# Kernel optimization log

Hardware: AMD Instinct MI355X
Metric: run time of the kernel (lower is better)

## Reference

```python
import jax, jax.numpy as jnp
import numpy as np

N_NODES, N_EDGES, N_GRAPHS = 20000, 640000, 256
D_IN, H1, H2, H3, L, H4, ED = 7, 128, 128, 64, 16, 64, 1


def _gat_conv(x, src, dst, edge_attr, W, att_s, att_d, We, att_e, b):
    """PyG GATConv (heads=1, concat=True, edge_dim=ED, add_self_loops=True,
    fill_value='mean' for self-loop edge attrs, negative_slope=0.2)."""
    n = x.shape[0]
    h = x @ W                                  # [N, F]
    a_s = h @ att_s                            # [N]
    a_d = h @ att_d                            # [N]
    # append self loops; self-loop edge attr = mean of edge attrs
    loop = jnp.arange(n)
    src_f = jnp.concatenate([src, loop])
    dst_f = jnp.concatenate([dst, loop])
    ea_mean = edge_attr.mean(axis=0, keepdims=True)
    ea = jnp.concatenate([edge_attr, jnp.broadcast_to(ea_mean, (n, edge_attr.shape[1]))], axis=0)
    a_e = (ea @ We) @ att_e                    # [E+N]
    logits = jax.nn.leaky_relu(a_s[src_f] + a_d[dst_f] + a_e, 0.2)
    # neighborhood softmax over incoming edges of each dst node
    m = jax.ops.segment_max(logits, dst_f, num_segments=n)
    ex = jnp.exp(logits - m[dst_f])
    denom = jax.ops.segment_sum(ex, dst_f, num_segments=n)
    alpha = ex / denom[dst_f]                  # [E+N]
    out = jax.ops.segment_sum(alpha[:, None] * h[src_f], dst_f, num_segments=n)
    return out + b


def _branch(x, edge_index, edge_col, params):
    src, dst = edge_index[0], edge_index[1]
    for p in params:  # fixed 3 layers
        x = jax.nn.elu(_gat_conv(x, src, dst, edge_col, *p))
        # dropout p=0.2 is identity in eval mode
    return x


def _mean_pool(x, batch, num_graphs):
    s = jax.ops.segment_sum(x, batch, num_segments=num_graphs)
    cnt = jax.ops.segment_sum(jnp.ones((x.shape[0],), x.dtype), batch, num_segments=num_graphs)
    return s / jnp.maximum(cnt, 1.0)[:, None]


def setup_inputs() -> dict:
    key = jax.random.key(0)
    ks = jax.random.split(key, 40)
    inp = {
        "x1": jax.random.normal(ks[0], (N_NODES, D_IN), jnp.float32),
        "x2": jax.random.normal(ks[1], (N_NODES, D_IN), jnp.float32),
        "edge_index1": jax.random.randint(ks[2], (2, N_EDGES), 0, N_NODES),
        "edge_index2": jax.random.randint(ks[3], (2, N_EDGES), 0, N_NODES),
        "batch1": jnp.sort(jax.random.randint(ks[4], (N_NODES,), 0, N_GRAPHS)),
        "batch2": jnp.sort(jax.random.randint(ks[5], (N_NODES,), 0, N_GRAPHS)),
        "x_norm2_1": jax.random.normal(ks[6], (N_GRAPHS, L), jnp.float32),
        "x_norm2_2": jax.random.normal(ks[7], (N_GRAPHS, L), jnp.float32),
        "edge_col1": jax.random.normal(ks[8], (N_EDGES, ED), jnp.float32),
        "edge_col2": jax.random.normal(ks[9], (N_EDGES, ED), jnp.float32),
    }
    dims = [(D_IN, H1), (H1, H2), (H2, H3)]
    k = 10
    for i, (fi, fo) in enumerate(dims, start=1):
        sc = 1.0 / np.sqrt(fi)
        inp[f"W{i}"] = jax.random.normal(ks[k], (fi, fo), jnp.float32) * sc; k += 1
        inp[f"as{i}"] = jax.random.normal(ks[k], (fo,), jnp.float32) * 0.1; k += 1
        inp[f"ad{i}"] = jax.random.normal(ks[k], (fo,), jnp.float32) * 0.1; k += 1
        inp[f"We{i}"] = jax.random.normal(ks[k], (ED, fo), jnp.float32); k += 1
        inp[f"ae{i}"] = jax.random.normal(ks[k], (fo,), jnp.float32) * 0.1; k += 1
        inp[f"b{i}"] = jnp.zeros((fo,), jnp.float32); k += 1
    inp["linW"] = jax.random.normal(ks[k], (H3 + L, H4), jnp.float32) * (1.0 / np.sqrt(H3 + L)); k += 1
    inp["linb"] = jnp.zeros((H4,), jnp.float32)
    return inp


def reference(x1, x2, edge_index1, edge_index2, batch1, batch2, x_norm2_1, x_norm2_2,
              edge_col1, edge_col2,
              W1, as1, ad1, We1, ae1, b1,
              W2, as2, ad2, We2, ae2, b2,
              W3, as3, ad3, We3, ae3, b3,
              linW, linb):
    params = [(W1, as1, ad1, We1, ae1, b1),
              (W2, as2, ad2, We2, ae2, b2),
              (W3, as3, ad3, We3, ae3, b3)]
    h1 = _branch(x1, edge_index1, edge_col1, params)
    h2 = _branch(x2, edge_index2, edge_col2, params)
    g1 = _mean_pool(h1, batch1, N_GRAPHS)
    g2 = _mean_pool(h2, batch2, N_GRAPHS)
    o1 = jnp.concatenate([g1, x_norm2_1], axis=1) @ linW + linb
    o2 = jnp.concatenate([g2, x_norm2_2], axis=1) @ linW + linb
    return (o1, o2)
```

## Files before the change

### kernel.cpp

```cpp
#include <hip/hip_runtime.h>
#include <hip/hip_bf16.h>
#include <hip/hip_fp16.h>

#define N_NODES 20000
#define N_EDGES 640000
#define N_GRAPHS 256
#define NBUCK 313
#define NBP 320
#define NA 160
#define NC 160
#define EPC 4000
#define DCAP 2560
#define CURP 16

typedef short bf16v __attribute__((ext_vector_type(8)));
typedef float f32x4 __attribute__((ext_vector_type(4)));
typedef float f32x2 __attribute__((ext_vector_type(2)));

__device__ __forceinline__ float leaky02(float x){ return x > 0.f ? x : 0.2f*x; }
__device__ __forceinline__ float eluf(float x){ return x > 0.f ? x : (__expf(x) - 1.f); }
__device__ __forceinline__ unsigned short f2bf(float x){
  __hip_bfloat16 t = __float2bfloat16(x);
  return *reinterpret_cast<unsigned short*>(&t);
}
__device__ __forceinline__ float bflo(unsigned int u){ return __uint_as_float(u << 16); }
__device__ __forceinline__ float bfhi(unsigned int u){ return __uint_as_float(u & 0xffff0000u); }
__device__ __forceinline__ void pkfma(f32x2& acc, f32x2 a, f32x2 b){
  asm volatile("v_pk_fma_f32 %0, %1, %2, %0" : "+v"(acc) : "v"(a), "v"(b));
}

__global__ __launch_bounds__(256) void binA_kernel(
    const int* __restrict__ ei0, const int* __restrict__ ei1,
    const float* __restrict__ ec0, const float* __restrict__ ec1,
    int* __restrict__ gcount, float* __restrict__ part)
{
  int b = blockIdx.y;
  const int* dstp = (b ? ei1 : ei0) + N_EDGES;
  const float* ec = b ? ec1 : ec0;
  __shared__ int hist[NBUCK];
  int tid = threadIdx.x;
  for (int j = tid; j < NBUCK; j += 256) hist[j] = 0;
  __syncthreads();
  float v = 0.f;
  for (int i = blockIdx.x*256 + tid; i < N_EDGES; i += NA*256){
    atomicAdd(&hist[dstp[i] >> 6], 1);
    v += ec[i];
  }
  __syncthreads();
  for (int j = tid; j < NBUCK; j += 256)
    if (hist[j]) atomicAdd(&gcount[b*NBP + j], hist[j]);
  for (int o = 32; o; o >>= 1) v += __shfl_down(v, o);
  __shared__ float wr[4];
  int lane = tid & 63, wv = tid >> 6;
  if (lane == 0) wr[wv] = v;
  __syncthreads();
  if (tid == 0) part[b*NA + blockIdx.x] = wr[0]+wr[1]+wr[2]+wr[3];
}

__global__ __launch_bounds__(512) void binB_kernel(
    const int* __restrict__ gcount, const float* __restrict__ part,
    const int* __restrict__ bat0, const int* __restrict__ bat1,
    const float* __restrict__ We1, const float* __restrict__ ae1,
    const float* __restrict__ We2, const float* __restrict__ ae2,
    const float* __restrict__ We3, const float* __restrict__ ae3,
    int* __restrict__ bcur, int* __restrict__ cbase,
    int* __restrict__ gb, float* __restrict__ scal, int* __restrict__ rowp)
{
  int b = blockIdx.x;
  int tid = threadIdx.x;
  if (b == 0){
    int wv = tid >> 6, lane = tid & 63;
    if (wv < 3){
      const float* We = wv==0 ? We1 : (wv==1 ? We2 : We3);
      const float* ae = wv==0 ? ae1 : (wv==1 ? ae2 : ae3);
      int F = (wv==2) ? 64 : 128;
      float s = 0.f;
      for (int i = lane; i < F; i += 64) s += We[i]*ae[i];
      for (int o = 32; o; o >>= 1) s += __shfl_down(s, o);
      if (lane == 0) scal[2+wv] = s;
    }
  }
  {
    float s = 0.f;
    for (int i = tid; i < NA; i += 512) s += part[b*NA + i];
    for (int o = 32; o; o >>= 1) s += __shfl_down(s, o);
    __shared__ float fr[8];
    if ((tid & 63) == 0) fr[tid >> 6] = s;
    __syncthreads();
    if (tid == 0){
      float t = 0.f;
      for (int i = 0; i < 8; ++i) t += fr[i];
      scal[b] = t;
    }
  }
  {
    const int* batch = b ? bat1 : bat0;
    int* gbb = gb + b*257;
    if (tid <= N_GRAPHS){
      int g = tid, lo = 0, hi = N_NODES;
      while (lo < hi){ int mid = (lo+hi) >> 1; if (batch[mid] < g) lo = mid+1; else hi = mid; }
      gbb[g] = lo;
    }
  }
  __shared__ int sc[512];
  int sz = (tid < NBUCK) ? gcount[b*NBP + tid] : 0;
  sc[tid] = sz;
  __syncthreads();
  for (int d = 1; d < 512; d <<= 1){
    int a2 = (tid >= d) ? sc[tid-d] : 0;
    __syncthreads();
    sc[tid] += a2;
    __syncthreads();
  }
  if (tid < NBUCK){
    int ecx = sc[tid] - sz;
    cbase[b*NBP + tid] = ecx;
    bcur[(b*NBUCK + tid)*CURP] = ecx;
  }
  if (tid == 0) rowp[b*(N_NODES+1) + N_NODES] = N_EDGES;
}

__global__ __launch_bounds__(256) void binC_kernel(
    const int* __restrict__ ei0, const int* __restrict__ ei1,
    const float* __restrict__ ec0, const float* __restrict__ ec1,
    int* __restrict__ bcur, uint2* __restrict__ stage)
{
  int b = blockIdx.y;
  const int* srcp = (b ? ei1 : ei0);
  const int* dstp = srcp + N_EDGES;
  const float* ec = b ? ec1 : ec0;
  int* bcurb = bcur + (size_t)b*NBUCK*CURP;
  uint2* stageb = stage + (size_t)b*N_EDGES;
  __shared__ uint2 recs[EPC];
  __shared__ int hist[NBUCK], rbase[NBUCK], rcur[NBUCK];
  int tid = threadIdx.x;
  for (int j = tid; j < NBUCK; j += 256){ hist[j] = 0; rcur[j] = 0; }
  __syncthreads();
  int e0 = blockIdx.x*EPC;
  for (int r = tid; r < EPC; r += 256){
    int i = e0 + r;
    int d = dstp[i];
    int bk = d >> 6;
    uint2 rec;
    rec.x = (unsigned)srcp[i] | ((unsigned)(d & 63) << 16);
    rec.y = ((unsigned)f2bf(ec[i]) << 16) | (unsigned)bk;
    recs[r] = rec;
    atomicAdd(&hist[bk], 1);
  }
  __syncthreads();
  for (int j = tid; j < NBUCK; j += 256){
    int h = hist[j];
    rbase[j] = h ? atomicAdd(&bcurb[j*CURP], h) : 0;
  }
  __syncthreads();
  for (int r = tid; r < EPC; r += 256){
    uint2 rc = recs[r];
    int bk = (int)(rc.y & 0xFFFFu);
    int p = rbase[bk] + atomicAdd(&rcur[bk], 1);
    stageb[p] = rc;
  }
}

__global__ __launch_bounds__(256) void binD_kernel(
    const uint2* __restrict__ stage, const int* __restrict__ gcount,
    const int* __restrict__ cbase,
    unsigned* __restrict__ final_, int* __restrict__ rowp)
{
  int b = blockIdx.y;
  int g = blockIdx.x;
  int tid = threadIdx.x;
  const uint2* stageb = stage + (size_t)b*N_EDGES;
  unsigned* finb = final_ + (size_t)b*N_EDGES;
  int* rowb = rowp + b*(N_NODES+1);
  int n = min(gcount[b*NBP + g], DCAP);
  int cb = cbase[b*NBP + g];
  __shared__ uint2 recs[DCAP];
  __shared__ int cnt64[64], cur64[64], off64[64];
  if (tid < 64) cnt64[tid] = 0;
  __syncthreads();
  for (int r = tid; r < n; r += 256){
    uint2 rc = stageb[cb + r];
    recs[r] = rc;
    atomicAdd(&cnt64[(rc.x >> 16) & 63], 1);
  }
  __syncthreads();
  if (tid == 0){
    int acc = 0;
    for (int dl = 0; dl < 64; ++dl){
      off64[dl] = acc; cur64[dl] = acc; acc += cnt64[dl];
    }
  }
  __syncthreads();
  int nd = min(64, N_NODES - g*64);
  if (tid < nd) rowb[g*64 + tid] = cb + off64[tid];
  for (int r = tid; r < n; r += 256){
    uint2 rc = recs[r];
    int dl = (rc.x >> 16) & 63;
    int p = atomicAdd(&cur64[dl], 1);
    finb[cb + p] = (rc.y & 0xFFFF0000u) | (rc.x & 0xFFFFu);
  }
}

template<int K, int F>
__global__ __launch_bounds__(256) void node_linear1_kernel(
    const float* __restrict__ x0, const float* __restrict__ x1,
    const float* __restrict__ W,
    const float* __restrict__ atts, const float* __restrict__ attd,
    unsigned short* __restrict__ hbAll, float* __restrict__ aSAll, float* __restrict__ aDAll)
{
  int b = blockIdx.y;
  const float* x = b ? x1 : x0;
  unsigned short* hb = hbAll + (size_t)b*N_NODES*128;
  float* a_s = aSAll + b*N_NODES;
  float* a_d = aDAll + b*N_NODES;
  constexpr int ROWS = 256 / F;
  __shared__ float Wl[K*F];
  __shared__ float xl[ROWS*K];
  __shared__ float swv[4], dwv[4];
  int tid = threadIdx.x;
  for (int i = tid; i < K*F; i += 256) Wl[i] = W[i];
  int f = tid % F;
  int lr = tid / F;
  float vs = atts[f], vd = attd[f];
  const int ntiles = (N_NODES + ROWS - 1)/ROWS;
  for (int t = blockIdx.x; t < ntiles; t += gridDim.x){
    int r0 = t*ROWS;
    __syncthreads();
    for (int i = tid; i < ROWS*K; i += 256){
      int r = i / K, k = i % K;
      int row = r0 + r;
      xl[i] = (row < N_NODES) ? x[row*K + k] : 0.f;
    }
    __syncthreads();
    float acc = 0.f;
    #pragma unroll
    for (int k = 0; k < K; ++k) acc += xl[lr*K + k] * Wl[k*F + f];
    int row = r0 + lr;
    if (row < N_NODES) hb[row*F + f] = f2bf(acc);
    float s = acc*vs, d = acc*vd;
    #pragma unroll
    for (int o = 32; o; o >>= 1){ s += __shfl_down(s, o); d += __shfl_down(d, o); }
    int wv = tid >> 6;
    if ((tid & 63) == 0){ swv[wv] = s; dwv[wv] = d; }
    __syncthreads();
    if (f == 0 && row < N_NODES){
      a_s[row] = swv[2*lr] + swv[2*lr+1];
      a_d[row] = dwv[2*lr] + dwv[2*lr+1];
    }
  }
}

template<int F>
__global__ __launch_bounds__(256) void gemm_mfma_kernel(
    const unsigned short* __restrict__ AAll, const float* __restrict__ W,
    const float* __restrict__ atts, const float* __restrict__ attd,
    unsigned short* __restrict__ hbAll, float* __restrict__ aSAll, float* __restrict__ aDAll)
{
  int b = blockIdx.y;
  const unsigned short* A = AAll + (size_t)b*N_NODES*128;
  unsigned short* hb = hbAll + (size_t)b*N_NODES*128;
  float* a_s = aSAll + b*N_NODES;
  float* a_d = aDAll + b*N_NODES;
  constexpr int NT = F/16;
  constexpr int KP = 136;
  __shared__ unsigned short Wb[F*KP];
  int tid = threadIdx.x;
  for (int idx = tid; idx < 128*F; idx += 256){
    int k = idx / F, col = idx % F;
    Wb[col*KP + k] = f2bf(W[idx]);
  }
  __syncthreads();
  int wave = tid >> 6, lane = tid & 63;
  int r0w = blockIdx.x*64 + wave*16;
  int arow = r0w + (lane & 15);
  bool av = arow < N_NODES;
  f32x4 acc[NT];
  #pragma unroll
  for (int nt = 0; nt < NT; ++nt) acc[nt] = 0.f;
  #pragma unroll
  for (int step = 0; step < 4; ++step){
    int kbase = step*32 + (lane>>4)*8;
    uint4 araw = av ? *reinterpret_cast<const uint4*>(&A[(size_t)arow*128 + kbase])
                    : make_uint4(0,0,0,0);
    bf16v af = __builtin_bit_cast(bf16v, araw);
    #pragma unroll
    for (int nt = 0; nt < NT; ++nt){
      uint4 braw = *reinterpret_cast<const uint4*>(&Wb[(nt*16 + (lane&15))*KP + kbase]);
      bf16v bfr = __builtin_bit_cast(bf16v, braw);
      acc[nt] = __builtin_amdgcn_mfma_f32_16x16x32_bf16(af, bfr, acc[nt], 0, 0, 0);
    }
  }
  float ps[4] = {0,0,0,0}, pd[4] = {0,0,0,0};
  #pragma unroll
  for (int nt = 0; nt < NT; ++nt){
    int col = nt*16 + (lane&15);
    float vs = atts[col], vd = attd[col];
    #pragma unroll
    for (int reg = 0; reg < 4; ++reg){
      int row = r0w + (lane>>4)*4 + reg;
      float v = acc[nt][reg];
      if (row < N_NODES) hb[(size_t)row*F + col] = f2bf(v);
      ps[reg] += v*vs;
      pd[reg] += v*vd;
    }
  }
  #pragma unroll
  for (int reg = 0; reg < 4; ++reg){
    float s = ps[reg], d = pd[reg];
    #pragma unroll
    for (int o = 1; o < 16; o <<= 1){ s += __shfl_xor(s, o); d += __shfl_xor(d, o); }
    int row = r0w + (lane>>4)*4 + reg;
    if ((lane & 15) == 0 && row < N_NODES){ a_s[row] = s; a_d[row] = d; }
  }
}

template<int F, bool W32>
__global__ __launch_bounds__(256) void aggregate_kernel(
    const unsigned short* __restrict__ hbAll,
    const float* __restrict__ aSAll, const float* __restrict__ aDAll,
    const unsigned* __restrict__ edgAll, const int* __restrict__ rowpAll,
    const float* __restrict__ scal, int l,
    const float* __restrict__ bias,
    float* __restrict__ out32All, unsigned short* __restrict__ outbAll)
{
  constexpr int PERL = F/16;
  constexpr int PERH = PERL/2;
  constexpr int RSH = (F == 128) ? 8 : 7;
  constexpr int SUBB = (F == 128) ? 16 : 8;
  int bid = blockIdx.x;
  int b = bid & 1;
  const unsigned short* hb = hbAll + (size_t)b*N_NODES*128;
  const float* a_s = aSAll + b*N_NODES;
  const float* a_d = aDAll + b*N_NODES;
  const unsigned* edges = edgAll + (size_t)b*N_EDGES;
  const int* rowp = rowpAll + b*(N_NODES+1);
  __shared__ uint2 sp[4][64];
  int wv = threadIdx.x >> 6;
  int lane = threadIdx.x & 63;
  int d = (bid >> 1)*4 + wv;
  if (d >= N_NODES) return;
  int sub = lane & 15, grp = lane >> 4;
  const char* hb2 = (const char*)hb + sub*SUBB;
  float c = scal[2+l];
  float ae_self = (scal[b] * (1.0f/N_EDGES)) * c;
  float add_ = a_d[d];
  float p_self = __expf(fminf(leaky02(a_s[d] + add_ + ae_self), 60.f));
  float dsum = 0.f;
  f32x2 acc[PERH];
  #pragma unroll
  for (int i = 0; i < PERH; ++i) acc[i] = (f32x2){0.f, 0.f};
  if (grp == 0){
    f32x2 pself2 = {p_self, p_self};
    if (PERL == 8){
      uint4 q = *reinterpret_cast<const uint4*>(hb2 + ((unsigned)d << RSH));
      pkfma(acc[0], (f32x2){bflo(q.x), bfhi(q.x)}, pself2);
      pkfma(acc[1], (f32x2){bflo(q.y), bfhi(q.y)}, pself2);
      pkfma(acc[2], (f32x2){bflo(q.z), bfhi(q.z)}, pself2);
      pkfma(acc[3], (f32x2){bflo(q.w), bfhi(q.w)}, pself2);
    } else {
      uint2 q = *reinterpret_cast<const uint2*>(hb2 + ((unsigned)d << RSH));
      pkfma(acc[0], (f32x2){bflo(q.x), bfhi(q.x)}, pself2);
      pkfma(acc[1], (f32x2){bflo(q.y), bfhi(q.y)}, pself2);
    }
  }
  int e0 = rowp[d], e1 = rowp[d+1];
  for (int ch = e0; ch < e1; ch += 64){
    int n = min(64, e1 - ch);
    unsigned off0 = 0;
    float p0 = 0.f;
    if (lane < n){
      unsigned e = edges[ch + lane];
      unsigned s0 = e & 0xFFFFu;
      p0 = __expf(fminf(leaky02(a_s[s0] + add_ + c*bfhi(e)), 60.f));
      off0 = s0 << RSH;
    }
    dsum += p0;
    sp[wv][lane] = make_uint2(off0, __float_as_uint(p0));
    #pragma unroll 4
    for (int e4 = 0; e4 < n; e4 += 16){
      uint2 r0 = sp[wv][e4 + grp];
      uint2 r1 = sp[wv][e4 + 4 + grp];
      uint2 r2 = sp[wv][e4 + 8 + grp];
      uint2 r3 = sp[wv][e4 + 12 + grp];
      f32x2 a0 = {__uint_as_float(r0.y), __uint_as_float(r0.y)};
      f32x2 a1 = {__uint_as_float(r1.y), __uint_as_float(r1.y)};
      f32x2 a2 = {__uint_as_float(r2.y), __uint_as_float(r2.y)};
      f32x2 a3 = {__uint_as_float(r3.y), __uint_as_float(r3.y)};
      if (PERL == 8){
        uint4 q0 = *reinterpret_cast<const uint4*>(hb2 + r0.x);
        uint4 q1 = *reinterpret_cast<const uint4*>(hb2 + r1.x);
        uint4 q2 = *reinterpret_cast<const uint4*>(hb2 + r2.x);
        uint4 q3 = *reinterpret_cast<const uint4*>(hb2 + r3.x);
        pkfma(acc[0], (f32x2){bflo(q0.x), bfhi(q0.x)}, a0);
        pkfma(acc[1], (f32x2){bflo(q0.y), bfhi(q0.y)}, a0);
        pkfma(acc[2], (f32x2){bflo(q0.z), bfhi(q0.z)}, a0);
        pkfma(acc[3], (f32x2){bflo(q0.w), bfhi(q0.w)}, a0);
        pkfma(acc[0], (f32x2){bflo(q1.x), bfhi(q1.x)}, a1);
        pkfma(acc[1], (f32x2){bflo(q1.y), bfhi(q1.y)}, a1);
        pkfma(acc[2], (f32x2){bflo(q1.z), bfhi(q1.z)}, a1);
        pkfma(acc[3], (f32x2){bflo(q1.w), bfhi(q1.w)}, a1);
        pkfma(acc[0], (f32x2){bflo(q2.x), bfhi(q2.x)}, a2);
        pkfma(acc[1], (f32x2){bflo(q2.y), bfhi(q2.y)}, a2);
        pkfma(acc[2], (f32x2){bflo(q2.z), bfhi(q2.z)}, a2);
        pkfma(acc[3], (f32x2){bflo(q2.w), bfhi(q2.w)}, a2);
        pkfma(acc[0], (f32x2){bflo(q3.x), bfhi(q3.x)}, a3);
        pkfma(acc[1], (f32x2){bflo(q3.y), bfhi(q3.y)}, a3);
        pkfma(acc[2], (f32x2){bflo(q3.z), bfhi(q3.z)}, a3);
        pkfma(acc[3], (f32x2){bflo(q3.w), bfhi(q3.w)}, a3);
      } else {
        uint2 q0 = *reinterpret_cast<const uint2*>(hb2 + r0.x);
        uint2 q1 = *reinterpret_cast<const uint2*>(hb2 + r1.x);
        uint2 q2 = *reinterpret_cast<const uint2*>(hb2 + r2.x);
        uint2 q3 = *reinterpret_cast<const uint2*>(hb2 + r3.x);
        pkfma(acc[0], (f32x2){bflo(q0.x), bfhi(q0.x)}, a0);
        pkfma(acc[1], (f32x2){bflo(q0.y), bfhi(q0.y)}, a0);
        pkfma(acc[0], (f32x2){bflo(q1.x), bfhi(q1.x)}, a1);
        pkfma(acc[1], (f32x2){bflo(q1.y), bfhi(q1.y)}, a1);
        pkfma(acc[0], (f32x2){bflo(q2.x), bfhi(q2.x)}, a2);
        pkfma(acc[1], (f32x2){bflo(q2.y), bfhi(q2.y)}, a2);
        pkfma(acc[0], (f32x2){bflo(q3.x), bfhi(q3.x)}, a3);
        pkfma(acc[1], (f32x2){bflo(q3.y), bfhi(q3.y)}, a3);
      }
    }
  }
  #pragma unroll
  for (int o = 32; o; o >>= 1) dsum += __shfl_xor(dsum, o);
  float denom = p_self + dsum;
  float inv = 1.0f/denom;
  float vv[PERL];
  #pragma unroll
  for (int i = 0; i < PERH; ++i){
    float v0 = acc[i].x, v1 = acc[i].y;
    v0 += __shfl_xor(v0, 16); v0 += __shfl_xor(v0, 32);
    v1 += __shfl_xor(v1, 16); v1 += __shfl_xor(v1, 32);
    vv[2*i]   = eluf(v0*inv + bias[PERL*sub + 2*i]);
    vv[2*i+1] = eluf(v1*inv + bias[PERL*sub + 2*i+1]);
  }
  if (grp == 0){
    if (W32){
      float* out32 = out32All + (size_t)b*N_NODES*64;
      *reinterpret_cast<float4*>(&out32[(size_t)d*64 + 4*sub]) = make_float4(vv[0],vv[1],vv[2],vv[3]);
    } else {
      unsigned short* outb = outbAll + (size_t)b*N_NODES*128;
      if (PERL == 8){
        uint4 o;
        o.x = (unsigned int)f2bf(vv[0]) | ((unsigned int)f2bf(vv[1]) << 16);
        o.y = (unsigned int)f2bf(vv[2]) | ((unsigned int)f2bf(vv[3]) << 16);
        o.z = (unsigned int)f2bf(vv[4]) | ((unsigned int)f2bf(vv[5]) << 16);
        o.w = (unsigned int)f2bf(vv[6]) | ((unsigned int)f2bf(vv[7]) << 16);
        *reinterpret_cast<uint4*>(&outb[(size_t)d*F + 8*sub]) = o;
      } else {
        uint2 o;
        o.x = (unsigned int)f2bf(vv[0]) | ((unsigned int)f2bf(vv[1]) << 16);
        o.y = (unsigned int)f2bf(vv[2]) | ((unsigned int)f2bf(vv[3]) << 16);
        *reinterpret_cast<uint2*>(&outb[(size_t)d*F + 4*sub]) = o;
      }
    }
  }
}

__global__ __launch_bounds__(256) void pool_final_kernel(
    const float* __restrict__ buf0, const int* __restrict__ gb,
    const float* __restrict__ xn0, const float* __restrict__ xn1,
    const float* __restrict__ linW, const float* __restrict__ linb,
    float* __restrict__ out)
{
  int bg = blockIdx.x;
  int b = bg >> 8, g = bg & 255;
  __shared__ float Wl[80*64];
  __shared__ float red[4][64];
  __shared__ float mf[64];
  int tid = threadIdx.x;
  for (int i = tid; i < 80*64; i += 256) Wl[i] = linW[i];
  const float* x = buf0 + (size_t)b*N_NODES*64;
  const int* gbb = gb + b*257;
  int s = gbb[g], e = gbb[g+1];
  int f = tid & 63, rg = tid >> 6;
  float acc = 0.f;
  for (int r = s + rg; r < e; r += 4) acc += x[r*64 + f];
  red[rg][f] = acc;
  __syncthreads();
  if (rg == 0)
    mf[f] = (red[0][f]+red[1][f]+red[2][f]+red[3][f]) / fmaxf((float)(e - s), 1.0f);
  __syncthreads();
  if (tid < 64){
    int j = tid;
    const float* xn = b ? xn1 : xn0;
    float a2 = linb[j];
    #pragma unroll 8
    for (int k = 0; k < 64; ++k) a2 += mf[k] * Wl[k*64 + j];
    #pragma unroll
    for (int k = 0; k < 16; ++k) a2 += xn[g*16+k] * Wl[(64+k)*64 + j];
    out[(size_t)(b*N_GRAPHS + g)*64 + j] = a2;
  }
}

extern "C" void kernel_launch(void* const* d_in, const int* in_sizes, int n_in,
                              void* d_out, int out_size, void* d_ws, size_t ws_size,
                              hipStream_t stream)
{
  const float* x1   = (const float*)d_in[0];
  const float* x2   = (const float*)d_in[1];
  const int*   ei1  = (const int*)d_in[2];
  const int*   ei2  = (const int*)d_in[3];
  const int*   bat1 = (const int*)d_in[4];
  const int*   bat2 = (const int*)d_in[5];
  const float* xn1  = (const float*)d_in[6];
  const float* xn2  = (const float*)d_in[7];
  const float* ec1  = (const float*)d_in[8];
  const float* ec2  = (const float*)d_in[9];
  const float* W[3]   = {(const float*)d_in[10], (const float*)d_in[16], (const float*)d_in[22]};
  const float* as_[3] = {(const float*)d_in[11], (const float*)d_in[17], (const float*)d_in[23]};
  const float* ad_[3] = {(const float*)d_in[12], (const float*)d_in[18], (const float*)d_in[24]};
  const float* We[3]  = {(const float*)d_in[13], (const float*)d_in[19], (const float*)d_in[25]};
  const float* ae[3]  = {(const float*)d_in[14], (const float*)d_in[20], (const float*)d_in[26]};
  const float* bb[3]  = {(const float*)d_in[15], (const float*)d_in[21], (const float*)d_in[27]};
  const float* linW = (const float*)d_in[28];
  const float* linb = (const float*)d_in[29];
  float* out = (float*)d_out;

  char* ws = (char*)d_ws;
  size_t off = 0;
  auto alloc = [&](size_t bytes)->char*{
    char* p = ws + off;
    off = (off + bytes + 255) & ~(size_t)255;
    return p;
  };
  unsigned short* hbA = (unsigned short*)alloc((size_t)2*N_NODES*128*2);
  unsigned short* hbB = (unsigned short*)alloc((size_t)2*N_NODES*128*2);
  float* buf0 = (float*)alloc((size_t)2*N_NODES*64*4);
  float* aS   = (float*)alloc((size_t)2*N_NODES*4);
  float* aD   = (float*)alloc((size_t)2*N_NODES*4);
  int* gcount = (int*)alloc((size_t)2*NBP*4);
  int* bcur   = (int*)alloc((size_t)2*NBUCK*CURP*4);
  int* cbase  = (int*)alloc((size_t)2*NBP*4);
  int* rowp   = (int*)alloc((size_t)2*(N_NODES+1)*4);
  uint2* stage = (uint2*)alloc((size_t)2*N_EDGES*8);
  unsigned* final_ = (unsigned*)alloc((size_t)2*N_EDGES*4);
  float* part = (float*)alloc((size_t)2*NA*4);
  int* gb     = (int*)alloc((size_t)2*257*4);
  float* scal = (float*)alloc(64);

  hipMemsetAsync(gcount, 0, (size_t)2*NBP*4, stream);
  binA_kernel<<<dim3(NA,2), 256, 0, stream>>>(ei1, ei2, ec1, ec2, gcount, part);
  binB_kernel<<<2, 512, 0, stream>>>(gcount, part, bat1, bat2,
      We[0], ae[0], We[1], ae[1], We[2], ae[2],
      bcur, cbase, gb, scal, rowp);
  binC_kernel<<<dim3(NC,2), 256, 0, stream>>>(ei1, ei2, ec1, ec2, bcur, stage);
  binD_kernel<<<dim3(NBUCK,2), 256, 0, stream>>>(stage, gcount, cbase, final_, rowp);

  const int AGG = 2*(N_NODES/4);

  node_linear1_kernel<7,128><<<dim3(1024,2), 256, 0, stream>>>(
      x1, x2, W[0], as_[0], ad_[0], hbA, aS, aD);
  aggregate_kernel<128,false><<<AGG, 256, 0, stream>>>(
      hbA, aS, aD, final_, rowp, scal, 0, bb[0], nullptr, hbB);

  gemm_mfma_kernel<128><<<dim3((N_NODES+63)/64,2), 256, 0, stream>>>(
      hbB, W[1], as_[1], ad_[1], hbA, aS, aD);
  aggregate_kernel<128,false><<<AGG, 256, 0, stream>>>(
      hbA, aS, aD, final_, rowp, scal, 1, bb[1], nullptr, hbB);

  gemm_mfma_kernel<64><<<dim3((N_NODES+63)/64,2), 256, 0, stream>>>(
      hbB, W[2], as_[2], ad_[2], hbA, aS, aD);
  aggregate_kernel<64,true><<<AGG, 256, 0, stream>>>(
      hbA, aS, aD, final_, rowp, scal, 2, bb[2], buf0, nullptr);

  pool_final_kernel<<<2*N_GRAPHS, 256, 0, stream>>>(
      buf0, gb, xn1, xn2, linW, linb, out);
}
```

Before: 211.9 us.

## Drop histogram pass by binning edges into fixed-capacity bucket slots

Removes the separate counting pass (binA) and prefix scan by giving each 64-node bucket a fixed slot of DCAP entries in the staging and final edge arrays. The bucket cursors are initialised to j*DCAP, and binC also accumulates the edge-attr partial sums. Row pointers become (start,end) int2 pairs, since buckets are no longer contiguous. This cuts one full read of the edge list and a memset plus launch. In exchange the buffers are padded, and any bucket with more than DCAP edges is silently truncated.

```diff
diff --git a/kernel.cpp b/kernel.cpp
--- a/kernel.cpp
+++ b/kernel.cpp
@@ -6,12 +6,11 @@
 #define N_EDGES 640000
 #define N_GRAPHS 256
 #define NBUCK 313
-#define NBP 320
-#define NA 160
 #define NC 160
 #define EPC 4000
 #define DCAP 2560
 #define CURP 16
+#define STAGEN ((size_t)NBUCK*DCAP)
 
 typedef short bf16v __attribute__((ext_vector_type(8)));
 typedef float f32x4 __attribute__((ext_vector_type(4)));
@@ -29,42 +28,71 @@
   asm volatile("v_pk_fma_f32 %0, %1, %2, %0" : "+v"(acc) : "v"(a), "v"(b));
 }
 
-__global__ __launch_bounds__(256) void binA_kernel(
+__global__ void init_kernel(int* __restrict__ bcur){
+  int i = blockIdx.x*256 + threadIdx.x;
+  if (i < 2*NBUCK){
+    int b = i / NBUCK, j = i % NBUCK;
+    bcur[((size_t)b*NBUCK + j)*CURP] = j*DCAP;
+  }
+}
+
+__global__ __launch_bounds__(256) void binC_kernel(
     const int* __restrict__ ei0, const int* __restrict__ ei1,
     const float* __restrict__ ec0, const float* __restrict__ ec1,
-    int* __restrict__ gcount, float* __restrict__ part)
+    int* __restrict__ bcur, uint2* __restrict__ stage, float* __restrict__ part)
 {
   int b = blockIdx.y;
-  const int* dstp = (b ? ei1 : ei0) + N_EDGES;
+  const int* srcp = (b ? ei1 : ei0);
+  const int* dstp = srcp + N_EDGES;
   const float* ec = b ? ec1 : ec0;
-  __shared__ int hist[NBUCK];
+  int* bcurb = bcur + (size_t)b*NBUCK*CURP;
+  uint2* stageb = stage + (size_t)b*STAGEN;
+  __shared__ uint2 recs[EPC];
+  __shared__ int hist[NBUCK], rbase[NBUCK], rcur[NBUCK];
   int tid = threadIdx.x;
-  for (int j = tid; j < NBUCK; j += 256) hist[j] = 0;
-  __syncthreads();
+  for (int j = tid; j < NBUCK; j += 256){ hist[j] = 0; rcur[j] = 0; }
+  __syncthreads();
+  int e0 = blockIdx.x*EPC;
   float v = 0.f;
-  for (int i = blockIdx.x*256 + tid; i < N_EDGES; i += NA*256){
-    atomicAdd(&hist[dstp[i] >> 6], 1);
-    v += ec[i];
-  }
-  __syncthreads();
-  for (int j = tid; j < NBUCK; j += 256)
-    if (hist[j]) atomicAdd(&gcount[b*NBP + j], hist[j]);
+  for (int r = tid; r < EPC; r += 256){
+    int i = e0 + r;
+    int d = dstp[i];
+    int bk = d >> 6;
+    uint2 rec;
+    rec.x = (unsigned)srcp[i] | ((unsigned)(d & 63) << 16);
+    float e = ec[i];
+    v += e;
+    rec.y = ((unsigned)f2bf(e) << 16) | (unsigned)bk;
+    recs[r] = rec;
+    atomicAdd(&hist[bk], 1);
+  }
+  __syncthreads();
+  for (int j = tid; j < NBUCK; j += 256){
+    int h = hist[j];
+    rbase[j] = h ? atomicAdd(&bcurb[j*CURP], h) : 0;
+  }
+  __syncthreads();
+  for (int r = tid; r < EPC; r += 256){
+    uint2 rc = recs[r];
+    int bk = (int)(rc.y & 0xFFFFu);
+    int p = rbase[bk] + atomicAdd(&rcur[bk], 1);
+    if (p < (bk + 1)*DCAP) stageb[p] = rc;
+  }
   for (int o = 32; o; o >>= 1) v += __shfl_down(v, o);
   __shared__ float wr[4];
   int lane = tid & 63, wv = tid >> 6;
   if (lane == 0) wr[wv] = v;
   __syncthreads();
-  if (tid == 0) part[b*NA + blockIdx.x] = wr[0]+wr[1]+wr[2]+wr[3];
+  if (tid == 0) part[b*NC + blockIdx.x] = wr[0]+wr[1]+wr[2]+wr[3];
 }
 
 __global__ __launch_bounds__(512) void binB_kernel(
-    const int* __restrict__ gcount, const float* __restrict__ part,
+    const float* __restrict__ part,
     const int* __restrict__ bat0, const int* __restrict__ bat1,
     const float* __restrict__ We1, const float* __restrict__ ae1,
     const float* __restrict__ We2, const float* __restrict__ ae2,
     const float* __restrict__ We3, const float* __restrict__ ae3,
-    int* __restrict__ bcur, int* __restrict__ cbase,
-    int* __restrict__ gb, float* __restrict__ scal, int* __restrict__ rowp)
+    int* __restrict__ gb, float* __restrict__ scal)
 {
   int b = blockIdx.x;
   int tid = threadIdx.x;
@@ -82,7 +110,7 @@
   }
   {
     float s = 0.f;
-    for (int i = tid; i < NA; i += 512) s += part[b*NA + i];
+    for (int i = tid; i < NC; i += 512) s += part[b*NC + i];
     for (int o = 32; o; o >>= 1) s += __shfl_down(s, o);
     __shared__ float fr[8];
     if ((tid & 63) == 0) fr[tid >> 6] = s;
@@ -102,78 +130,20 @@
       gbb[g] = lo;
     }
   }
-  __shared__ int sc[512];
-  int sz = (tid < NBUCK) ? gcount[b*NBP + tid] : 0;
-  sc[tid] = sz;
-  __syncthreads();
-  for (int d = 1; d < 512; d <<= 1){
-    int a2 = (tid >= d) ? sc[tid-d] : 0;
-    __syncthreads();
-    sc[tid] += a2;
-    __syncthreads();
-  }
-  if (tid < NBUCK){
-    int ecx = sc[tid] - sz;
-    cbase[b*NBP + tid] = ecx;
-    bcur[(b*NBUCK + tid)*CURP] = ecx;
-  }
-  if (tid == 0) rowp[b*(N_NODES+1) + N_NODES] = N_EDGES;
-}
-
-__global__ __launch_bounds__(256) void binC_kernel(
-    const int* __restrict__ ei0, const int* __restrict__ ei1,
-    const float* __restrict__ ec0, const float* __restrict__ ec1,
-    int* __restrict__ bcur, uint2* __restrict__ stage)
-{
-  int b = blockIdx.y;
-  const int* srcp = (b ? ei1 : ei0);
-  const int* dstp = srcp + N_EDGES;
-  const float* ec = b ? ec1 : ec0;
-  int* bcurb = bcur + (size_t)b*NBUCK*CURP;
-  uint2* stageb = stage + (size_t)b*N_EDGES;
-  __shared__ uint2 recs[EPC];
-  __shared__ int hist[NBUCK], rbase[NBUCK], rcur[NBUCK];
-  int tid = threadIdx.x;
-  for (int j = tid; j < NBUCK; j += 256){ hist[j] = 0; rcur[j] = 0; }
-  __syncthreads();
-  int e0 = blockIdx.x*EPC;
-  for (int r = tid; r < EPC; r += 256){
-    int i = e0 + r;
-    int d = dstp[i];
-    int bk = d >> 6;
-    uint2 rec;
-    rec.x = (unsigned)srcp[i] | ((unsigned)(d & 63) << 16);
-    rec.y = ((unsigned)f2bf(ec[i]) << 16) | (unsigned)bk;
-    recs[r] = rec;
-    atomicAdd(&hist[bk], 1);
-  }
-  __syncthreads();
-  for (int j = tid; j < NBUCK; j += 256){
-    int h = hist[j];
-    rbase[j] = h ? atomicAdd(&bcurb[j*CURP], h) : 0;
-  }
-  __syncthreads();
-  for (int r = tid; r < EPC; r += 256){
-    uint2 rc = recs[r];
-    int bk = (int)(rc.y & 0xFFFFu);
-    int p = rbase[bk] + atomicAdd(&rcur[bk], 1);
-    stageb[p] = rc;
-  }
 }
 
 __global__ __launch_bounds__(256) void binD_kernel(
-    const uint2* __restrict__ stage, const int* __restrict__ gcount,
-    const int* __restrict__ cbase,
-    unsigned* __restrict__ final_, int* __restrict__ rowp)
+    const uint2* __restrict__ stage, const int* __restrict__ bcur,
+    unsigned* __restrict__ final_, int2* __restrict__ rowp2)
 {
   int b = blockIdx.y;
   int g = blockIdx.x;
   int tid = threadIdx.x;
-  const uint2* stageb = stage + (size_t)b*N_EDGES;
-  unsigned* finb = final_ + (size_t)b*N_EDGES;
-  int* rowb = rowp + b*(N_NODES+1);
-  int n = min(gcount[b*NBP + g], DCAP);
-  int cb = cbase[b*NBP + g];
+  const uint2* stageb = stage + (size_t)b*STAGEN;
+  unsigned* finb = final_ + (size_t)b*STAGEN;
+  int2* rowb = rowp2 + (size_t)b*N_NODES;
+  int cb = g*DCAP;
+  int n = min(bcur[((size_t)b*NBUCK + g)*CURP] - cb, DCAP);
   __shared__ uint2 recs[DCAP];
   __shared__ int cnt64[64], cur64[64], off64[64];
   if (tid < 64) cnt64[tid] = 0;
@@ -192,7 +162,8 @@
   }
   __syncthreads();
   int nd = min(64, N_NODES - g*64);
-  if (tid < nd) rowb[g*64 + tid] = cb + off64[tid];
+  if (tid < nd)
+    rowb[g*64 + tid] = make_int2(cb + off64[tid], cb + off64[tid] + cnt64[tid]);
   for (int r = tid; r < n; r += 256){
     uint2 rc = recs[r];
     int dl = (rc.x >> 16) & 63;
@@ -318,7 +289,7 @@
 __global__ __launch_bounds__(256) void aggregate_kernel(
     const unsigned short* __restrict__ hbAll,
     const float* __restrict__ aSAll, const float* __restrict__ aDAll,
-    const unsigned* __restrict__ edgAll, const int* __restrict__ rowpAll,
+    const unsigned* __restrict__ edgAll, const int2* __restrict__ rowp2All,
     const float* __restrict__ scal, int l,
     const float* __restrict__ bias,
     float* __restrict__ out32All, unsigned short* __restrict__ outbAll)
@@ -332,8 +303,8 @@
   const unsigned short* hb = hbAll + (size_t)b*N_NODES*128;
   const float* a_s = aSAll + b*N_NODES;
   const float* a_d = aDAll + b*N_NODES;
-  const unsigned* edges = edgAll + (size_t)b*N_EDGES;
-  const int* rowp = rowpAll + b*(N_NODES+1);
+  const unsigned* edges = edgAll + (size_t)b*STAGEN;
+  const int2* rowp2 = rowp2All + (size_t)b*N_NODES;
   __shared__ uint2 sp[4][64];
   int wv = threadIdx.x >> 6;
   int lane = threadIdx.x & 63;
@@ -363,7 +334,8 @@
       pkfma(acc[1], (f32x2){bflo(q.y), bfhi(q.y)}, pself2);
     }
   }
-  int e0 = rowp[d], e1 = rowp[d+1];
+  int2 r2 = rowp2[d];
+  int e0 = r2.x, e1 = r2.y;
   for (int ch = e0; ch < e1; ch += 64){
     int n = min(64, e1 - ch);
     unsigned off0 = 0;
@@ -380,16 +352,16 @@
     for (int e4 = 0; e4 < n; e4 += 16){
       uint2 r0 = sp[wv][e4 + grp];
       uint2 r1 = sp[wv][e4 + 4 + grp];
-      uint2 r2 = sp[wv][e4 + 8 + grp];
+      uint2 rr2 = sp[wv][e4 + 8 + grp];
       uint2 r3 = sp[wv][e4 + 12 + grp];
       f32x2 a0 = {__uint_as_float(r0.y), __uint_as_float(r0.y)};
       f32x2 a1 = {__uint_as_float(r1.y), __uint_as_float(r1.y)};
-      f32x2 a2 = {__uint_as_float(r2.y), __uint_as_float(r2.y)};
+      f32x2 a2 = {__uint_as_float(rr2.y), __uint_as_float(rr2.y)};
       f32x2 a3 = {__uint_as_float(r3.y), __uint_as_float(r3.y)};
       if (PERL == 8){
         uint4 q0 = *reinterpret_cast<const uint4*>(hb2 + r0.x);
         uint4 q1 = *reinterpret_cast<const uint4*>(hb2 + r1.x);
-        uint4 q2 = *reinterpret_cast<const uint4*>(hb2 + r2.x);
+        uint4 q2 = *reinterpret_cast<const uint4*>(hb2 + rr2.x);
         uint4 q3 = *reinterpret_cast<const uint4*>(hb2 + r3.x);
         pkfma(acc[0], (f32x2){bflo(q0.x), bfhi(q0.x)}, a0);
         pkfma(acc[1], (f32x2){bflo(q0.y), bfhi(q0.y)}, a0);
@@ -410,7 +382,7 @@
       } else {
         uint2 q0 = *reinterpret_cast<const uint2*>(hb2 + r0.x);
         uint2 q1 = *reinterpret_cast<const uint2*>(hb2 + r1.x);
-        uint2 q2 = *reinterpret_cast<const uint2*>(hb2 + r2.x);
+        uint2 q2 = *reinterpret_cast<const uint2*>(hb2 + rr2.x);
         uint2 q3 = *reinterpret_cast<const uint2*>(hb2 + r3.x);
         pkfma(acc[0], (f32x2){bflo(q0.x), bfhi(q0.x)}, a0);
         pkfma(acc[1], (f32x2){bflo(q0.y), bfhi(q0.y)}, a0);
@@ -531,40 +503,36 @@
   float* buf0 = (float*)alloc((size_t)2*N_NODES*64*4);
   float* aS   = (float*)alloc((size_t)2*N_NODES*4);
   float* aD   = (float*)alloc((size_t)2*N_NODES*4);
-  int* gcount = (int*)alloc((size_t)2*NBP*4);
   int* bcur   = (int*)alloc((size_t)2*NBUCK*CURP*4);
-  int* cbase  = (int*)alloc((size_t)2*NBP*4);
-  int* rowp   = (int*)alloc((size_t)2*(N_NODES+1)*4);
-  uint2* stage = (uint2*)alloc((size_t)2*N_EDGES*8);
-  unsigned* final_ = (unsigned*)alloc((size_t)2*N_EDGES*4);
-  float* part = (float*)alloc((size_t)2*NA*4);
+  int2* rowp2 = (int2*)alloc((size_t)2*N_NODES*8);
+  uint2* stage = (uint2*)alloc((size_t)2*STAGEN*8);
+  unsigned* final_ = (unsigned*)alloc((size_t)2*STAGEN*4);
+  float* part = (float*)alloc((size_t)2*NC*4);
   int* gb     = (int*)alloc((size_t)2*257*4);
   float* scal = (float*)alloc(64);
 
-  hipMemsetAsync(gcount, 0, (size_t)2*NBP*4, stream);
-  binA_kernel<<<dim3(NA,2), 256, 0, stream>>>(ei1, ei2, ec1, ec2, gcount, part);
-  binB_kernel<<<2, 512, 0, stream>>>(gcount, part, bat1, bat2,
-      We[0], ae[0], We[1], ae[1], We[2], ae[2],
-      bcur, cbase, gb, scal, rowp);
-  binC_kernel<<<dim3(NC,2), 256, 0, stream>>>(ei1, ei2, ec1, ec2, bcur, stage);
-  binD_kernel<<<dim3(NBUCK,2), 256, 0, stream>>>(stage, gcount, cbase, final_, rowp);
+  init_kernel<<<(2*NBUCK + 255)/256, 256, 0, stream>>>(bcur);
+  binC_kernel<<<dim3(NC,2), 256, 0, stream>>>(ei1, ei2, ec1, ec2, bcur, stage, part);
+  binB_kernel<<<2, 512, 0, stream>>>(part, bat1, bat2,
+      We[0], ae[0], We[1], ae[1], We[2], ae[2], gb, scal);
+  binD_kernel<<<dim3(NBUCK,2), 256, 0, stream>>>(stage, bcur, final_, rowp2);
 
   const int AGG = 2*(N_NODES/4);
 
   node_linear1_kernel<7,128><<<dim3(1024,2), 256, 0, stream>>>(
       x1, x2, W[0], as_[0], ad_[0], hbA, aS, aD);
   aggregate_kernel<128,false><<<AGG, 256, 0, stream>>>(
-      hbA, aS, aD, final_, rowp, scal, 0, bb[0], nullptr, hbB);
+      hbA, aS, aD, final_, rowp2, scal, 0, bb[0], nullptr, hbB);
 
   gemm_mfma_kernel<128><<<dim3((N_NODES+63)/64,2), 256, 0, stream>>>(
       hbB, W[1], as_[1], ad_[1], hbA, aS, aD);
   aggregate_kernel<128,false><<<AGG, 256, 0, stream>>>(
-      hbA, aS, aD, final_, rowp, scal, 1, bb[1], nullptr, hbB);
+      hbA, aS, aD, final_, rowp2, scal, 1, bb[1], nullptr, hbB);
 
   gemm_mfma_kernel<64><<<dim3((N_NODES+63)/64,2), 256, 0, stream>>>(
       hbB, W[2], as_[2], ad_[2], hbA, aS, aD);
   aggregate_kernel<64,true><<<AGG, 256, 0, stream>>>(
-      hbA, aS, aD, final_, rowp, scal, 2, bb[2], buf0, nullptr);
+      hbA, aS, aD, final_, rowp2, scal, 2, bb[2], buf0, nullptr);
 
   pool_final_kernel<<<2*N_GRAPHS, 256, 0, stream>>>(
       buf0, gb, xn1, xn2, linW, linb, out);
```

Result: faster. 200.0 us (-5.6%).
